# Optimization experiments

Hardware: AMD Instinct MI355X
Metric: run time of the kernel (lower is better)

The kernel has to match this reference:

```python
import jax, jax.numpy as jnp
import numpy as np


def binarize_weight(w):
    # clip to [-1,1], sign in forward, straight-through gradient of clip in backward
    clipped = jnp.clip(w, -1.0, 1.0)
    rounded = jnp.sign(clipped)
    return clipped + jax.lax.stop_gradient(rounded - clipped)


def setup_inputs() -> dict:
    key = jax.random.key(0)
    k1, k2 = jax.random.split(key)
    d_in, filters = 4096, 4096
    n_tokens = 8192
    stdv = 1.0 / np.sqrt(d_in)
    x = jax.random.normal(k1, (n_tokens, d_in), dtype=jnp.float32)
    w = jax.random.normal(k2, (d_in, filters), dtype=jnp.float32) * stdv
    b = jnp.zeros((filters,), dtype=jnp.float32)
    return {"x": x, "w": w, "b": b}


def reference(x, w, b):
    # [N, d_in] @ binarized [d_in, filters] + bias
    out = jnp.matmul(x, binarize_weight(w))
    return out + b
```

## Files before the change

### kernel.cpp

```cpp
#include <hip/hip_runtime.h>
#include <hip/hip_bf16.h>
#include <cstdint>

typedef __attribute__((ext_vector_type(8))) short bf16x8;
typedef __attribute__((ext_vector_type(4))) float f32x4;
typedef __attribute__((ext_vector_type(4))) int   i32x4;

static constexpr int Mdim = 8192;
static constexpr int Kdim = 4096;
static constexpr int Ndim = 4096;
static constexpr int BM = 128, BN = 128;

__device__ __forceinline__ void async_copy16(const void* g, void* l) {
  __builtin_amdgcn_global_load_lds(
      (const __attribute__((address_space(1))) void*)g,
      (__attribute__((address_space(3))) void*)l, 16, 0, 0);
}

__global__ __launch_bounds__(256) void quant_x_kernel(const float* __restrict__ x,
                                                      int8_t* __restrict__ xq,
                                                      float* __restrict__ srow) {
  const int tid = threadIdx.x;
  const int row = blockIdx.x * 8 + (tid >> 5);
  const int l   = tid & 31;
  const float* xr = x + (size_t)row * Kdim;
  float4 v[32];
  float m = 0.f;
  #pragma unroll
  for (int j = 0; j < 32; ++j) {
    v[j] = *reinterpret_cast<const float4*>(xr + (size_t)(j * 32 + l) * 4);
    m = fmaxf(m, fmaxf(fmaxf(fabsf(v[j].x), fabsf(v[j].y)),
                       fmaxf(fabsf(v[j].z), fabsf(v[j].w))));
  }
  #pragma unroll
  for (int s = 16; s >= 1; s >>= 1) m = fmaxf(m, __shfl_xor(m, s, 64));
  const float rs = (m > 0.f) ? (127.0f / m) : 0.f;
  if (l == 0) srow[row] = m * (1.0f / 127.0f);
  uint32_t* xq32 = reinterpret_cast<uint32_t*>(xq + (size_t)row * Kdim);
  #pragma unroll
  for (int j = 0; j < 32; ++j) {
    int a0 = (int)rintf(v[j].x * rs), a1 = (int)rintf(v[j].y * rs);
    int a2 = (int)rintf(v[j].z * rs), a3 = (int)rintf(v[j].w * rs);
    uint32_t p = (uint32_t)(a0 & 255) | ((uint32_t)(a1 & 255) << 8) |
                 ((uint32_t)(a2 & 255) << 16) | ((uint32_t)(a3 & 255) << 24);
    xq32[j * 32 + l] = p;
  }
}

__global__ __launch_bounds__(256) void sign_w_kernel(const float* __restrict__ w,
                                                     int8_t* __restrict__ wsT) {
  __shared__ int8_t t[64 * 68];
  const int bid = blockIdx.x;
  const int k0 = (bid & 63) * 64;
  const int n0 = (bid >> 6) * 64;
  const int tid = threadIdx.x;
  #pragma unroll
  for (int r = 0; r < 4; ++r) {
    int c  = r * 256 + tid;
    int k  = c >> 4;
    int n4 = (c & 15) * 4;
    float4 v = *reinterpret_cast<const float4*>(w + (size_t)(k0 + k) * Ndim + n0 + n4);
    int s0 = (v.x > 0.f) - (v.x < 0.f);
    int s1 = (v.y > 0.f) - (v.y < 0.f);
    int s2 = (v.z > 0.f) - (v.z < 0.f);
    int s3 = (v.w > 0.f) - (v.w < 0.f);
    uint32_t p = (uint32_t)(s0 & 255) | ((uint32_t)(s1 & 255) << 8) |
                 ((uint32_t)(s2 & 255) << 16) | ((uint32_t)(s3 & 255) << 24);
    *reinterpret_cast<uint32_t*>(&t[k * 68 + n4]) = p;
  }
  __syncthreads();
  const int n  = tid & 63;
  const int ck = (tid >> 6) * 16;
  union { int8_t b[16]; uint4 u; } o;
  #pragma unroll
  for (int j = 0; j < 16; ++j) o.b[j] = t[(ck + j) * 68 + n];
  *reinterpret_cast<uint4*>(wsT + (size_t)(n0 + n) * Kdim + k0 + ck) = o.u;
}

__global__ __launch_bounds__(256) void gemm_i8_kernel(const int8_t* __restrict__ A,
                                                      const int8_t* __restrict__ Bt,
                                                      const float* __restrict__ srow,
                                                      const float* __restrict__ bias,
                                                      float* __restrict__ out) {
  __shared__ int8_t sA[BM * 64];
  __shared__ int8_t sB[BN * 64];
  const int tid  = threadIdx.x;
  const int bn   = blockIdx.x, bm = blockIdx.y;
  const int lane = tid & 63;
  const int wave = tid >> 6;
  const int wm   = (wave & 1) * 64;
  const int wn   = (wave >> 1) * 64;
  const int lr   = lane & 15;
  const int quad = lane >> 4;

  const int c0 = tid, c1 = tid + 256;
  const int row0 = c0 >> 2, col0 = (c0 & 3) * 16;
  const int row1 = c1 >> 2, col1 = (c1 & 3) * 16;
  const int8_t* gA0 = A  + (size_t)(bm * BM + row0) * Kdim + col0;
  const int8_t* gA1 = A  + (size_t)(bm * BM + row1) * Kdim + col1;
  const int8_t* gB0 = Bt + (size_t)(bn * BN + row0) * Kdim + col0;
  const int8_t* gB1 = Bt + (size_t)(bn * BN + row1) * Kdim + col1;

  i32x4 acc[4][4] = {};

  for (int k0 = 0; k0 < Kdim; k0 += 64) {
    async_copy16(gA0 + k0, &sA[c0 * 16]);
    async_copy16(gA1 + k0, &sA[c1 * 16]);
    async_copy16(gB0 + k0, &sB[c0 * 16]);
    async_copy16(gB1 + k0, &sB[c1 * 16]);
    __syncthreads();

    i32x4 af[4], bf[4];
    #pragma unroll
    for (int i = 0; i < 4; ++i)
      af[i] = *reinterpret_cast<const i32x4*>(&sA[(wm + i * 16 + lr) * 64 + quad * 16]);
    #pragma unroll
    for (int j = 0; j < 4; ++j)
      bf[j] = *reinterpret_cast<const i32x4*>(&sB[(wn + j * 16 + lr) * 64 + quad * 16]);
    #pragma unroll
    for (int i = 0; i < 4; ++i)
      #pragma unroll
      for (int j = 0; j < 4; ++j)
        acc[i][j] = __builtin_amdgcn_mfma_i32_16x16x64_i8(af[i], bf[j], acc[i][j], 0, 0, 0);
    __syncthreads();
  }

  float bv[4];
  #pragma unroll
  for (int j = 0; j < 4; ++j) bv[j] = bias[bn * BN + wn + j * 16 + lr];
  #pragma unroll
  for (int i = 0; i < 4; ++i) {
    const int rowb = bm * BM + wm + i * 16 + quad * 4;
    float sv[4];
    #pragma unroll
    for (int r = 0; r < 4; ++r) sv[r] = srow[rowb + r];
    #pragma unroll
    for (int j = 0; j < 4; ++j) {
      const int col = bn * BN + wn + j * 16 + lr;
      float* o = out + (size_t)rowb * Ndim + col;
      #pragma unroll
      for (int r = 0; r < 4; ++r)
        o[(size_t)r * Ndim] = (float)acc[i][j][r] * sv[r] + bv[j];
    }
  }
}

__global__ __launch_bounds__(256) void gemm_fused_kernel(const float* __restrict__ X,
                                                         const float* __restrict__ W,
                                                         const float* __restrict__ bias,
                                                         float* __restrict__ out) {
  __shared__ __hip_bfloat16 sA[BM * 32];
  __shared__ __hip_bfloat16 sB[BN * 32];
  const int tid  = threadIdx.x;
  const int bn   = blockIdx.x, bm = blockIdx.y;
  const int lane = tid & 63;
  const int wave = tid >> 6;
  const int wm   = (wave & 1) * 64;
  const int wn   = (wave >> 1) * 64;
  const int lr   = lane & 15;
  const int quad = lane >> 4;

  f32x4 acc[4][4] = {};

  for (int k0 = 0; k0 < Kdim; k0 += 32) {
    #pragma unroll
    for (int r = 0; r < 2; ++r) {
      int c = r * 256 + tid;
      int row = c >> 2, col = (c & 3) * 8;
      const float4* p = reinterpret_cast<const float4*>(X + (size_t)(bm * BM + row) * Kdim + k0 + col);
      float4 v0 = p[0], v1 = p[1];
      float va[8] = {v0.x, v0.y, v0.z, v0.w, v1.x, v1.y, v1.z, v1.w};
      union { __hip_bfloat16 h[8]; uint4 u; } oa;
      #pragma unroll
      for (int u2 = 0; u2 < 8; ++u2) oa.h[u2] = __float2bfloat16(va[u2]);
      *reinterpret_cast<uint4*>(&sA[c * 8]) = oa.u;

      int kl = c >> 4, n8 = (c & 15) * 8;
      const float4* q = reinterpret_cast<const float4*>(W + (size_t)(k0 + kl) * Ndim + bn * BN + n8);
      float4 w0 = q[0], w1 = q[1];
      float wv[8] = {w0.x, w0.y, w0.z, w0.w, w1.x, w1.y, w1.z, w1.w};
      #pragma unroll
      for (int u2 = 0; u2 < 8; ++u2) {
        float sg = (wv[u2] > 0.f) ? 1.f : ((wv[u2] < 0.f) ? -1.f : 0.f);
        sB[(n8 + u2) * 32 + kl] = __float2bfloat16(sg);
      }
    }
    __syncthreads();

    bf16x8 af[4], bf[4];
    #pragma unroll
    for (int i = 0; i < 4; ++i)
      af[i] = *reinterpret_cast<const bf16x8*>(&sA[(wm + i * 16 + lr) * 32 + quad * 8]);
    #pragma unroll
    for (int j = 0; j < 4; ++j)
      bf[j] = *reinterpret_cast<const bf16x8*>(&sB[(wn + j * 16 + lr) * 32 + quad * 8]);
    #pragma unroll
    for (int i = 0; i < 4; ++i)
      #pragma unroll
      for (int j = 0; j < 4; ++j)
        acc[i][j] = __builtin_amdgcn_mfma_f32_16x16x32_bf16(af[i], bf[j], acc[i][j], 0, 0, 0);
    __syncthreads();
  }

  float bv[4];
  #pragma unroll
  for (int j = 0; j < 4; ++j) bv[j] = bias[bn * BN + wn + j * 16 + lr];
  #pragma unroll
  for (int i = 0; i < 4; ++i) {
    const size_t rowb = (size_t)(bm * BM + wm + i * 16 + quad * 4);
    #pragma unroll
    for (int j = 0; j < 4; ++j) {
      const int col = bn * BN + wn + j * 16 + lr;
      float* o = out + rowb * Ndim + col;
      #pragma unroll
      for (int r = 0; r < 4; ++r)
        o[(size_t)r * Ndim] = acc[i][j][r] + bv[j];
    }
  }
}

extern "C" void kernel_launch(void* const* d_in, const int* in_sizes, int n_in,
                              void* d_out, int out_size, void* d_ws, size_t ws_size,
                              hipStream_t stream) {
  const float* x = (const float*)d_in[0];
  const float* w = (const float*)d_in[1];
  const float* b = (const float*)d_in[2];
  float* out = (float*)d_out;

  const size_t xq_bytes = (size_t)Mdim * Kdim;
  const size_t wt_bytes = (size_t)Ndim * Kdim;
  const size_t sr_bytes = (size_t)Mdim * sizeof(float);
  const size_t need = xq_bytes + wt_bytes + sr_bytes;

  if (ws_size >= need) {
    int8_t* xq  = (int8_t*)d_ws;
    int8_t* wsT = (int8_t*)((char*)d_ws + xq_bytes);
    float* srow = (float*)((char*)d_ws + xq_bytes + wt_bytes);
    quant_x_kernel<<<Mdim / 8, 256, 0, stream>>>(x, xq, srow);
    sign_w_kernel<<<(Kdim / 64) * (Ndim / 64), 256, 0, stream>>>(w, wsT);
    gemm_i8_kernel<<<dim3(Ndim / BN, Mdim / BM), 256, 0, stream>>>(xq, wsT, srow, b, out);
  } else {
    gemm_fused_kernel<<<dim3(Ndim / BN, Mdim / BM), 256, 0, stream>>>(x, w, b, out);
  }
}
```

Baseline: 423.4 us.

## Switch int8 GEMM to 32x32x32 MFMA with BK=128 and XOR-swizzled LDS

Rewrites the int8 GEMM main loop to use 32x32x32 i8 MFMA tiles (2x2 per wave) instead of 16x16x64 (4x4), doubles the K slab per iteration to 128 to halve barrier count, and applies an XOR swizzle on 16-byte column groups in LDS to avoid bank conflicts on fragment reads. Launch bounds now request 4 blocks per CU. The epilogue is adapted to the 32x32 accumulator layout. Larger LDS tiles (32KB per block) may limit occupancy, and there is still no double buffering.

```diff
diff --git a/kernel.cpp b/kernel.cpp
--- a/kernel.cpp
+++ b/kernel.cpp
@@ -5,11 +5,13 @@
 typedef __attribute__((ext_vector_type(8))) short bf16x8;
 typedef __attribute__((ext_vector_type(4))) float f32x4;
 typedef __attribute__((ext_vector_type(4))) int   i32x4;
+typedef __attribute__((ext_vector_type(16))) int  i32x16;
 
 static constexpr int Mdim = 8192;
 static constexpr int Kdim = 4096;
 static constexpr int Ndim = 4096;
 static constexpr int BM = 128, BN = 128;
+static constexpr int BKB = 128;
 
 __device__ __forceinline__ void async_copy16(const void* g, void* l) {
   __builtin_amdgcn_global_load_lds(
@@ -77,70 +79,84 @@
   *reinterpret_cast<uint4*>(wsT + (size_t)(n0 + n) * Kdim + k0 + ck) = o.u;
 }
 
-__global__ __launch_bounds__(256) void gemm_i8_kernel(const int8_t* __restrict__ A,
-                                                      const int8_t* __restrict__ Bt,
-                                                      const float* __restrict__ srow,
-                                                      const float* __restrict__ bias,
-                                                      float* __restrict__ out) {
-  __shared__ int8_t sA[BM * 64];
-  __shared__ int8_t sB[BN * 64];
+__global__ __launch_bounds__(256, 4) void gemm_i8_kernel(const int8_t* __restrict__ A,
+                                                         const int8_t* __restrict__ Bt,
+                                                         const float* __restrict__ srow,
+                                                         const float* __restrict__ bias,
+                                                         float* __restrict__ out) {
+  __shared__ int8_t sA[BM * BKB];
+  __shared__ int8_t sB[BN * BKB];
   const int tid  = threadIdx.x;
   const int bn   = blockIdx.x, bm = blockIdx.y;
   const int lane = tid & 63;
   const int wave = tid >> 6;
   const int wm   = (wave & 1) * 64;
   const int wn   = (wave >> 1) * 64;
-  const int lr   = lane & 15;
-  const int quad = lane >> 4;
-
-  const int c0 = tid, c1 = tid + 256;
-  const int row0 = c0 >> 2, col0 = (c0 & 3) * 16;
-  const int row1 = c1 >> 2, col1 = (c1 & 3) * 16;
-  const int8_t* gA0 = A  + (size_t)(bm * BM + row0) * Kdim + col0;
-  const int8_t* gA1 = A  + (size_t)(bm * BM + row1) * Kdim + col1;
-  const int8_t* gB0 = Bt + (size_t)(bn * BN + row0) * Kdim + col0;
-  const int8_t* gB1 = Bt + (size_t)(bn * BN + row1) * Kdim + col1;
-
-  i32x4 acc[4][4] = {};
-
-  for (int k0 = 0; k0 < Kdim; k0 += 64) {
-    async_copy16(gA0 + k0, &sA[c0 * 16]);
-    async_copy16(gA1 + k0, &sA[c1 * 16]);
-    async_copy16(gB0 + k0, &sB[c0 * 16]);
-    async_copy16(gB1 + k0, &sB[c1 * 16]);
-    __syncthreads();
-
-    i32x4 af[4], bf[4];
-    #pragma unroll
-    for (int i = 0; i < 4; ++i)
-      af[i] = *reinterpret_cast<const i32x4*>(&sA[(wm + i * 16 + lr) * 64 + quad * 16]);
-    #pragma unroll
-    for (int j = 0; j < 4; ++j)
-      bf[j] = *reinterpret_cast<const i32x4*>(&sB[(wn + j * 16 + lr) * 64 + quad * 16]);
-    #pragma unroll
-    for (int i = 0; i < 4; ++i)
-      #pragma unroll
-      for (int j = 0; j < 4; ++j)
-        acc[i][j] = __builtin_amdgcn_mfma_i32_16x16x64_i8(af[i], bf[j], acc[i][j], 0, 0, 0);
-    __syncthreads();
-  }
-
-  float bv[4];
-  #pragma unroll
-  for (int j = 0; j < 4; ++j) bv[j] = bias[bn * BN + wn + j * 16 + lr];
-  #pragma unroll
-  for (int i = 0; i < 4; ++i) {
-    const int rowb = bm * BM + wm + i * 16 + quad * 4;
-    float sv[4];
-    #pragma unroll
-    for (int r = 0; r < 4; ++r) sv[r] = srow[rowb + r];
-    #pragma unroll
-    for (int j = 0; j < 4; ++j) {
-      const int col = bn * BN + wn + j * 16 + lr;
-      float* o = out + (size_t)rowb * Ndim + col;
-      #pragma unroll
-      for (int r = 0; r < 4; ++r)
-        o[(size_t)r * Ndim] = (float)acc[i][j][r] * sv[r] + bv[j];
+  const int m    = lane & 31;
+  const int h    = lane >> 5;
+  const int em   = m & 7;
+
+  const int8_t* gAp[4];
+  const int8_t* gBp[4];
+  #pragma unroll
+  for (int p = 0; p < 4; ++p) {
+    int s  = tid + 256 * p;
+    int r  = s >> 3;
+    int cg = (s & 7) ^ (r & 7);
+    gAp[p] = A  + (size_t)(bm * BM + r) * Kdim + cg * 16;
+    gBp[p] = Bt + (size_t)(bn * BN + r) * Kdim + cg * 16;
+  }
+
+  i32x16 acc[2][2] = {};
+
+  for (int k0 = 0; k0 < Kdim; k0 += BKB) {
+    #pragma unroll
+    for (int p = 0; p < 4; ++p) {
+      async_copy16(gAp[p] + k0, &sA[(tid + 256 * p) * 16]);
+      async_copy16(gBp[p] + k0, &sB[(tid + 256 * p) * 16]);
+    }
+    __syncthreads();
+
+    #pragma unroll
+    for (int ks = 0; ks < 4; ++ks) {
+      const int cx = ((ks * 2 + h) ^ em) * 16;
+      i32x4 af[2], bf[2];
+      #pragma unroll
+      for (int i = 0; i < 2; ++i)
+        af[i] = *reinterpret_cast<const i32x4*>(&sA[(wm + i * 32 + m) * BKB + cx]);
+      #pragma unroll
+      for (int j = 0; j < 2; ++j)
+        bf[j] = *reinterpret_cast<const i32x4*>(&sB[(wn + j * 32 + m) * BKB + cx]);
+      #pragma unroll
+      for (int i = 0; i < 2; ++i)
+        #pragma unroll
+        for (int j = 0; j < 2; ++j)
+          acc[i][j] = __builtin_amdgcn_mfma_i32_32x32x32_i8(af[i], bf[j], acc[i][j], 0, 0, 0);
+    }
+    __syncthreads();
+  }
+
+  float bv[2];
+  #pragma unroll
+  for (int j = 0; j < 2; ++j) bv[j] = bias[bn * BN + wn + j * 32 + m];
+  #pragma unroll
+  for (int i = 0; i < 2; ++i) {
+    const int base_row = bm * BM + wm + i * 32 + 4 * h;
+    #pragma unroll
+    for (int gg = 0; gg < 4; ++gg) {
+      float sv[4];
+      #pragma unroll
+      for (int rr = 0; rr < 4; ++rr) sv[rr] = srow[base_row + gg * 8 + rr];
+      #pragma unroll
+      for (int j = 0; j < 2; ++j) {
+        const int col = bn * BN + wn + j * 32 + m;
+        #pragma unroll
+        for (int rr = 0; rr < 4; ++rr) {
+          const int reg = gg * 4 + rr;
+          out[(size_t)(base_row + gg * 8 + rr) * Ndim + col] =
+              (float)acc[i][j][reg] * sv[rr] + bv[j];
+        }
+      }
     }
   }
 }
```

After: 409.0 us. 1.04x faster.
